# Kernel tuning notes

Hardware: AMD Instinct MI355X
Metric: run time of the kernel (lower is better)

## Reference

```python
import jax, jax.numpy as jnp
import numpy as np

B = 2048      # number of binary mixtures
NPM = 30      # atoms per molecule
N = B * NPM   # total nodes per side
EPM = 120     # directed edges per molecule
IN_DIM = 74
H = 128
NC = 2


def setup_inputs() -> dict:
    key = jax.random.key(0)
    ks = jax.random.split(key, 24)
    rng = np.random.default_rng(0)
    off = np.repeat(np.arange(B, dtype=np.int64) * NPM, EPM)
    mk_idx = lambda: jnp.asarray((rng.integers(0, NPM, B * EPM) + off).astype(np.int32))

    def lin(k, fi, fo):
        return (jax.random.normal(k, (fi, fo), jnp.float32) / np.sqrt(fi)).astype(jnp.float32)

    inp = {
        'h1': jax.random.normal(ks[0], (N, IN_DIM), jnp.float32),
        'h2': jax.random.normal(ks[1], (N, IN_DIM), jnp.float32),
        'solv1_x': jax.random.uniform(ks[2], (B,), jnp.float32),
        'inter_hb': jax.random.uniform(ks[3], (B,), jnp.float32),
        'intra_hb1': jax.random.uniform(ks[4], (B,), jnp.float32),
        'intra_hb2': jax.random.uniform(ks[5], (B,), jnp.float32),
        'Wg1': lin(ks[6], IN_DIM, H), 'bg1': jnp.zeros((H,), jnp.float32),
        'Wg2': lin(ks[7], H, H), 'bg2': jnp.zeros((H,), jnp.float32),
        'Wp': lin(ks[8], H, H), 'bp': jnp.zeros((H,), jnp.float32),
        'We1': lin(ks[9], 1, 32), 'be1': jnp.zeros((32,), jnp.float32),
        'We2': lin(ks[10], 32, H * H), 'be2': jnp.zeros((H * H,), jnp.float32),
        'bnn': jnp.zeros((H,), jnp.float32),
        'Wih': lin(ks[11], H, 3 * H), 'bih': jnp.zeros((3 * H,), jnp.float32),
        'Whh': lin(ks[12], H, 3 * H), 'bhh': jnp.zeros((3 * H,), jnp.float32),
        'Wcl1': lin(ks[13], 2 * H, H), 'bcl1': jnp.zeros((H,), jnp.float32),
        'Wcl2': lin(ks[14], H, H), 'bcl2': jnp.zeros((H,), jnp.float32),
        'Wcl3': lin(ks[15], H, NC), 'bcl3': jnp.zeros((NC,), jnp.float32),
        'src1': mk_idx(), 'dst1': mk_idx(), 'src2': mk_idx(), 'dst2': mk_idx(),
    }
    return inp


def _graphconv(x, src, dst, W, b, n):
    # DGL GraphConv, norm='both': D_in^{-1/2} A D_out^{-1/2} X W + b
    ones = jnp.ones(src.shape[0], x.dtype)
    d_out = jnp.maximum(jax.ops.segment_sum(ones, src, num_segments=n), 1.0)
    d_in = jnp.maximum(jax.ops.segment_sum(ones, dst, num_segments=n), 1.0)
    m = (x * jax.lax.rsqrt(d_out)[:, None])[src]
    agg = jax.ops.segment_sum(m, dst, num_segments=n)
    return (agg * jax.lax.rsqrt(d_in)[:, None]) @ W + b


def _gru_step(x, h, Wih, bih, Whh, bhh):
    gi = x @ Wih + bih
    gh = h @ Whh + bhh
    ir, iz, ih = jnp.split(gi, 3, axis=-1)
    hr, hz, hn = jnp.split(gh, 3, axis=-1)
    r = jax.nn.sigmoid(ir + hr)
    z = jax.nn.sigmoid(iz + hz)
    n = jnp.tanh(ih + r * hn)
    return (1.0 - z) * n + z * h


def _forward(h1, h2, solv1_x, inter_hb, intra_hb1, intra_hb2,
             Wg1, bg1, Wg2, bg2, Wp, bp, We1, be1, We2, be2, bnn,
             Wih, bih, Whh, bhh, Wcl1, bcl1, Wcl2, bcl2, Wcl3, bcl3,
             src1, dst1, src2, dst2):
    # shared GraphConv layers on both molecule graphs
    t1 = jax.nn.relu(_graphconv(h1, src1, dst1, Wg1, bg1, N))
    t1 = jax.nn.relu(_graphconv(t1, src1, dst1, Wg2, bg2, N))
    t2 = jax.nn.relu(_graphconv(h2, src2, dst2, Wg1, bg1, N))
    t2 = jax.nn.relu(_graphconv(t2, src2, dst2, Wg2, bg2, N))
    # dgl.mean_nodes: per-molecule mean (uniform NPM nodes per molecule)
    hg1 = t1.reshape(B, NPM, H).mean(axis=1) * solv1_x[:, None]
    hg2 = t2.reshape(B, NPM, H).mean(axis=1) * (1.0 - solv1_x)[:, None]
    x = jnp.concatenate([hg1, hg2], axis=0)  # (2B, H)

    # empty_solvsys: inter edges i<->i+B (both dirs) then self-loops
    ar = jnp.arange(B, dtype=jnp.int32)
    ss = jnp.concatenate([ar, ar + B, ar, ar + B])
    sd = jnp.concatenate([ar + B, ar, ar, ar + B])
    ef = jnp.concatenate([inter_hb, inter_hb, intra_hb1, intra_hb2])[:, None]  # (4B,1)

    # MPNNconv: project, NNConv(sum) + GRU, 1 message-passing step
    x = jax.nn.relu(x @ Wp + bp)
    hstate = x
    for _ in range(1):
        w = (jax.nn.relu(ef @ We1 + be1) @ We2 + be2).reshape(-1, H, H)  # (4B,H,H)
        msg = jnp.einsum('ed,edf->ef', x[ss], w)
        agg = jax.ops.segment_sum(msg, sd, num_segments=2 * B) + bnn
        x = _gru_step(jax.nn.relu(agg), hstate, Wih, bih, Whh, bhh)
        hstate = x

    hg = jnp.concatenate([x[:B], x[B:]], axis=1)  # (B, 2H)
    o = jax.nn.relu(hg @ Wcl1 + bcl1)
    o = jax.nn.relu(o @ Wcl2 + bcl2)
    return o @ Wcl3 + bcl3


def reference(h1, h2, solv1_x, inter_hb, intra_hb1, intra_hb2,
              Wg1, bg1, Wg2, bg2, Wp, bp, We1, be1, We2, be2, bnn,
              Wih, bih, Whh, bhh, Wcl1, bcl1, Wcl2, bcl2, Wcl3, bcl3,
              src1, dst1, src2, dst2):
    return _forward(h1, h2, solv1_x, inter_hb, intra_hb1, intra_hb2,
                    Wg1, bg1, Wg2, bg2, Wp, bp, We1, be1, We2, be2, bnn,
                    Wih, bih, Whh, bhh, Wcl1, bcl1, Wcl2, bcl2, Wcl3, bcl3,
                    src1, dst1, src2, dst2)
```

## Files before the change

kernel.cpp:

```cpp
#include <hip/hip_runtime.h>
#include <hip/hip_bf16.h>
#include <math.h>

#define B2    2048
#define NPM   30
#define EPM   120

typedef __attribute__((ext_vector_type(8))) short short8;
typedef __attribute__((ext_vector_type(4))) float f32x4;

__device__ __forceinline__ ushort f2bf(float x) {
  unsigned u = __float_as_uint(x);
  return (ushort)((u + 0x7FFFu + ((u >> 16) & 1u)) >> 16);
}
__device__ __forceinline__ float bf2f(ushort h) {
  return __uint_as_float(((unsigned)h) << 16);
}

__device__ __forceinline__ int swz128(int r, int kb) { return r * 128 + (kb ^ ((r & 7) << 4)); }
__device__ __forceinline__ int swz256(int r, int kb) { return r * 256 + (kb ^ ((r & 15) << 4)); }

struct PrepDescs {
  const float* W[8];
  ushort* hi[8];
  ushort* lo[8];
  int Kreal[8], Kpad[8], N[8];
  int blk0[9];
};

__global__ __launch_bounds__(256) void prep_all_kernel(PrepDescs d)
{
  int b = blockIdx.x;
  int di = 0;
  #pragma unroll
  for (int j = 1; j < 8; ++j) if (b >= d.blk0[j]) di = j;
  int idx = (b - d.blk0[di]) * 256 + threadIdx.x;
  int Kp8 = d.Kpad[di] >> 3;
  int tot = d.N[di] * Kp8;
  if (idx >= tot) return;
  int n = idx / Kp8;
  int k8 = (idx - n * Kp8) << 3;
  const float* W = d.W[di];
  ushort* hi = d.hi[di];
  ushort* lo = d.lo[di];
  int Kreal = d.Kreal[di], Kpad = d.Kpad[di], N = d.N[di];
  #pragma unroll
  for (int j = 0; j < 8; ++j) {
    int k = k8 + j;
    float x = (k < Kreal) ? W[(long)k * N + n] : 0.f;
    ushort h = f2bf(x);
    hi[(long)n * Kpad + k] = h;
    lo[(long)n * Kpad + k] = f2bf(x - bf2f(h));
  }
}

__global__ __launch_bounds__(256) void prep_we2_kernel(
    const float* __restrict__ We2, ushort* __restrict__ hi, ushort* __restrict__ lo)
{
  int idx = blockIdx.x * 256 + threadIdx.x;
  int k = idx >> 11;
  int rem = idx & 2047;
  int n = rem >> 4;
  int d8 = (rem & 15) << 3;
  #pragma unroll
  for (int j = 0; j < 8; ++j) {
    int d = d8 + j;
    float x = We2[k * 16384 + d * 128 + n];
    ushort h = f2bf(x);
    hi[k * 16384 + n * 128 + d] = h;
    lo[k * 16384 + n * 128 + d] = f2bf(x - bf2f(h));
  }
}

__global__ __launch_bounds__(256, 4) void grufuse_kernel(
    const float* __restrict__ aggA, const float* __restrict__ aggB,
    const float* __restrict__ zb, const float* __restrict__ bnn,
    const float* __restrict__ xp,
    const ushort* __restrict__ Wihh, const ushort* __restrict__ Wihl,
    const float* __restrict__ bih,
    const ushort* __restrict__ Whhh, const ushort* __restrict__ Whhl,
    const float* __restrict__ bhh,
    float* __restrict__ xnew)
{
  __shared__ __align__(16) char A1h[8192], A1l[8192];
  __shared__ __align__(16) char A2h[8192], A2l[8192];
  __shared__ __align__(16) char Bh[4096], Bl[4096];
  const int tid = threadIdx.x;
  const int w = tid >> 6, l = tid & 63;
  const int rt = blockIdx.x >> 2;
  const int qt = blockIdx.x & 3;
  const long rowBase = (long)rt * 32;
  const int rw = w & 1;
  const int cs = w >> 1;
  const int ar = rw * 16 + (l & 15);
  const int crow = rw * 16 + ((l >> 4) << 2);

  #pragma unroll
  for (int q = 0; q < 4; ++q) {
    int t = tid + 256 * q;
    int r = t >> 5, k4 = (t & 31) << 2;
    long gr = rowBase + r;
    long i = (gr < B2) ? gr : (gr - B2);
    float4 za = *(const float4*)&zb[i * 128 + k4];
    float4 zc = *(const float4*)&zb[(i + B2) * 128 + k4];
    float4 bn = *(const float4*)&bnn[k4];
    const float* ap = (gr < B2) ? &aggA[i * 128 + k4] : &aggB[i * 128 + k4];
    float4 ag = *(const float4*)ap;
    float4 xv;
    xv.x = fmaxf(ag.x + za.x + zc.x + bn.x, 0.f);
    xv.y = fmaxf(ag.y + za.y + zc.y + bn.y, 0.f);
    xv.z = fmaxf(ag.z + za.z + zc.z + bn.z, 0.f);
    xv.w = fmaxf(ag.w + za.w + zc.w + bn.w, 0.f);
    ushort4 h4, l4;
    h4.x = f2bf(xv.x); l4.x = f2bf(xv.x - bf2f(h4.x));
    h4.y = f2bf(xv.y); l4.y = f2bf(xv.y - bf2f(h4.y));
    h4.z = f2bf(xv.z); l4.z = f2bf(xv.z - bf2f(h4.z));
    h4.w = f2bf(xv.w); l4.w = f2bf(xv.w - bf2f(h4.w));
    *(ushort4*)(A1h + swz256(r, k4 * 2)) = h4;
    *(ushort4*)(A1l + swz256(r, k4 * 2)) = l4;
    float4 pv = *(const float4*)&xp[gr * 128 + k4];
    h4.x = f2bf(pv.x); l4.x = f2bf(pv.x - bf2f(h4.x));
    h4.y = f2bf(pv.y); l4.y = f2bf(pv.y - bf2f(h4.y));
    h4.z = f2bf(pv.z); l4.z = f2bf(pv.z - bf2f(h4.z));
    h4.w = f2bf(pv.w); l4.w = f2bf(pv.w - bf2f(h4.w));
    *(ushort4*)(A2h + swz256(r, k4 * 2)) = h4;
    *(ushort4*)(A2l + swz256(r, k4 * 2)) = l4;
  }
  __syncthreads();

  f32x4 rg = (f32x4){0,0,0,0}, zg = (f32x4){0,0,0,0};

  for (int gate = 0; gate < 3; ++gate) {
    f32x4 gi = (f32x4){0,0,0,0}, gh = (f32x4){0,0,0,0};
    for (int src = 0; src < 2; ++src) {
      const ushort* Wh = src ? Whhh : Wihh;
      const ushort* Wl = src ? Whhl : Wihl;
      const char* Ah = src ? A2h : A1h;
      const char* Al = src ? A2l : A1l;
      for (int k0 = 0; k0 < 128; k0 += 64) {
        __syncthreads();
        {
          int n = tid >> 3, k8 = (tid & 7) << 3;
          long wrow = (long)(gate * 128 + qt * 32 + n);
          *(uint4*)(Bh + swz128(n, k8 * 2)) = *(const uint4*)&Wh[wrow * 128 + k0 + k8];
          *(uint4*)(Bl + swz128(n, k8 * 2)) = *(const uint4*)&Wl[wrow * 128 + k0 + k8];
        }
        __syncthreads();
        f32x4 a = (src == 0) ? gi : gh;
        #pragma unroll
        for (int ks = 0; ks < 2; ++ks) {
          const int ko = ks * 32 + (l >> 4) * 8;
          short8 ah  = *(const short8*)(Ah + swz256(ar, (k0 + ko) * 2));
          short8 al8 = *(const short8*)(Al + swz256(ar, (k0 + ko) * 2));
          const int c = cs * 16 + (l & 15);
          short8 bh  = *(const short8*)(Bh + swz128(c, ko * 2));
          short8 bl8 = *(const short8*)(Bl + swz128(c, ko * 2));
          a = __builtin_amdgcn_mfma_f32_16x16x32_bf16(al8, bh, a, 0, 0, 0);
          a = __builtin_amdgcn_mfma_f32_16x16x32_bf16(ah, bl8, a, 0, 0, 0);
          a = __builtin_amdgcn_mfma_f32_16x16x32_bf16(ah, bh, a, 0, 0, 0);
        }
        if (src == 0) gi = a; else gh = a;
      }
    }
    int cg = qt * 32 + cs * 16 + (l & 15);
    float bi = bih[gate * 128 + cg], bh2 = bhh[gate * 128 + cg];
    #pragma unroll
    for (int i = 0; i < 4; ++i) {
      float a = gi[i] + bi;
      float b = gh[i] + bh2;
      if (gate == 0) {
        rg[i] = 1.f / (1.f + expf(-(a + b)));
      } else if (gate == 1) {
        zg[i] = 1.f / (1.f + expf(-(a + b)));
      } else {
        float ng = tanhf(a + rg[i] * b);
        long row = rowBase + crow + i;
        float h = xp[row * 128 + cg];
        xnew[row * 128 + cg] = (1.f - zg[i]) * ng + zg[i] * h;
      }
    }
  }
}

__global__ __launch_bounds__(256) void xpzb_kernel(
    const float* __restrict__ xcat,
    const ushort* __restrict__ Wph, const ushort* __restrict__ Wpl,
    const float* __restrict__ bp,
    const ushort* __restrict__ be2h, const ushort* __restrict__ be2l,
    float* __restrict__ xp, float* __restrict__ zb)
{
  __shared__ __align__(16) char AhB[16384], AlB[16384];
  __shared__ __align__(16) char BhB[16384], BlB[16384];
  const int tid = threadIdx.x;
  const int w = tid >> 6, l = tid & 63;
  const long rowBase = (long)blockIdx.x * 64;
  const int ar = w * 16 + (l & 15);
  const int crow = w * 16 + ((l >> 4) << 2);

  #pragma unroll
  for (int q = 0; q < 8; ++q) {
    int t = tid + 256 * q;
    int r = t >> 5, k4 = (t & 31) << 2;
    float4 v = *(const float4*)&xcat[(rowBase + r) * 128 + k4];
    ushort4 h4, l4;
    h4.x = f2bf(v.x); l4.x = f2bf(v.x - bf2f(h4.x));
    h4.y = f2bf(v.y); l4.y = f2bf(v.y - bf2f(h4.y));
    h4.z = f2bf(v.z); l4.z = f2bf(v.z - bf2f(h4.z));
    h4.w = f2bf(v.w); l4.w = f2bf(v.w - bf2f(h4.w));
    *(ushort4*)(AhB + swz256(r, k4 * 2)) = h4;
    *(ushort4*)(AlB + swz256(r, k4 * 2)) = l4;
  }
  __syncthreads();

  f32x4 acc[8];
  #pragma unroll
  for (int fc = 0; fc < 8; ++fc) acc[fc] = (f32x4){0.f, 0.f, 0.f, 0.f};
  for (int k0 = 0; k0 < 128; k0 += 64) {
    #pragma unroll
    for (int q = 0; q < 4; ++q) {
      int lin = tid + 256 * q;
      int n = lin >> 3, k8 = (lin & 7) << 3;
      *(uint4*)(BhB + swz128(n, k8 * 2)) = *(const uint4*)&Wph[n * 128 + k0 + k8];
      *(uint4*)(BlB + swz128(n, k8 * 2)) = *(const uint4*)&Wpl[n * 128 + k0 + k8];
    }
    __syncthreads();
    #pragma unroll
    for (int ks = 0; ks < 2; ++ks) {
      const int ko = ks * 32 + (l >> 4) * 8;
      short8 ah  = *(const short8*)(AhB + swz256(ar, (k0 + ko) * 2));
      short8 al8 = *(const short8*)(AlB + swz256(ar, (k0 + ko) * 2));
      #pragma unroll
      for (int fc = 0; fc < 8; ++fc) {
        const int c = fc * 16 + (l & 15);
        short8 bh  = *(const short8*)(BhB + swz128(c, ko * 2));
        short8 bl8 = *(const short8*)(BlB + swz128(c, ko * 2));
        acc[fc] = __builtin_amdgcn_mfma_f32_16x16x32_bf16(al8, bh, acc[fc], 0, 0, 0);
        acc[fc] = __builtin_amdgcn_mfma_f32_16x16x32_bf16(ah, bl8, acc[fc], 0, 0, 0);
        acc[fc] = __builtin_amdgcn_mfma_f32_16x16x32_bf16(ah, bh, acc[fc], 0, 0, 0);
      }
    }
    __syncthreads();
  }

  #pragma unroll
  for (int fc = 0; fc < 8; ++fc) {
    int col = fc * 16 + (l & 15);
    float bv = bp[col];
    #pragma unroll
    for (int i = 0; i < 4; ++i) {
      int lr = crow + i;
      float v = fmaxf(acc[fc][i] + bv, 0.f);
      xp[(rowBase + lr) * 128 + col] = v;
      ushort h = f2bf(v);
      *(ushort*)(AhB + swz256(lr, col * 2)) = h;
      *(ushort*)(AlB + swz256(lr, col * 2)) = f2bf(v - bf2f(h));
    }
  }

  #pragma unroll
  for (int fc = 0; fc < 8; ++fc) acc[fc] = (f32x4){0.f, 0.f, 0.f, 0.f};
  for (int k0 = 0; k0 < 128; k0 += 64) {
    __syncthreads();
    #pragma unroll
    for (int q = 0; q < 4; ++q) {
      int lin = tid + 256 * q;
      int n = lin >> 3, k8 = (lin & 7) << 3;
      *(uint4*)(BhB + swz128(n, k8 * 2)) = *(const uint4*)&be2h[n * 128 + k0 + k8];
      *(uint4*)(BlB + swz128(n, k8 * 2)) = *(const uint4*)&be2l[n * 128 + k0 + k8];
    }
    __syncthreads();
    #pragma unroll
    for (int ks = 0; ks < 2; ++ks) {
      const int ko = ks * 32 + (l >> 4) * 8;
      short8 ah  = *(const short8*)(AhB + swz256(ar, (k0 + ko) * 2));
      short8 al8 = *(const short8*)(AlB + swz256(ar, (k0 + ko) * 2));
      #pragma unroll
      for (int fc = 0; fc < 8; ++fc) {
        const int c = fc * 16 + (l & 15);
        short8 bh  = *(const short8*)(BhB + swz128(c, ko * 2));
        short8 bl8 = *(const short8*)(BlB + swz128(c, ko * 2));
        acc[fc] = __builtin_amdgcn_mfma_f32_16x16x32_bf16(al8, bh, acc[fc], 0, 0, 0);
        acc[fc] = __builtin_amdgcn_mfma_f32_16x16x32_bf16(ah, bl8, acc[fc], 0, 0, 0);
        acc[fc] = __builtin_amdgcn_mfma_f32_16x16x32_bf16(ah, bh, acc[fc], 0, 0, 0);
      }
    }
  }
  #pragma unroll
  for (int fc = 0; fc < 8; ++fc) {
    int col = fc * 16 + (l & 15);
    #pragma unroll
    for (int i = 0; i < 4; ++i) {
      int lr = crow + i;
      zb[(rowBase + lr) * 128 + col] = acc[fc][i];
    }
  }
}

__global__ __launch_bounds__(256) void cls_kernel(
    const float* __restrict__ xnew,
    const ushort* __restrict__ W1h, const ushort* __restrict__ W1l,
    const float* __restrict__ b1,
    const ushort* __restrict__ W2h, const ushort* __restrict__ W2l,
    const float* __restrict__ b2,
    const float* __restrict__ Wcl3, const float* __restrict__ bcl3,
    float* __restrict__ out)
{
  __shared__ __align__(16) char O1h[16384], O1l[16384];
  __shared__ __align__(16) char AhB[8192], AlB[8192];
  __shared__ __align__(16) char BhB[16384], BlB[16384];
  const int tid = threadIdx.x;
  const int w = tid >> 6, l = tid & 63;
  const long rowBase = (long)blockIdx.x * 64;
  const int ar = w * 16 + (l & 15);
  const int crow = w * 16 + ((l >> 4) << 2);

  f32x4 acc[8];
  #pragma unroll
  for (int fc = 0; fc < 8; ++fc) acc[fc] = (f32x4){0.f, 0.f, 0.f, 0.f};
  for (int k0 = 0; k0 < 256; k0 += 64) {
    const float* Ab = (k0 < 128) ? xnew : (xnew + (long)B2 * 128);
    const int kc = k0 & 127;
    #pragma unroll
    for (int q = 0; q < 4; ++q) {
      int lin = tid + 256 * q;
      int r = lin >> 4, k4 = (lin & 15) << 2;
      float4 v = *(const float4*)&Ab[(rowBase + r) * 128 + kc + k4];
      ushort4 h4, l4;
      h4.x = f2bf(v.x); l4.x = f2bf(v.x - bf2f(h4.x));
      h4.y = f2bf(v.y); l4.y = f2bf(v.y - bf2f(h4.y));
      h4.z = f2bf(v.z); l4.z = f2bf(v.z - bf2f(h4.z));
      h4.w = f2bf(v.w); l4.w = f2bf(v.w - bf2f(h4.w));
      *(ushort4*)(AhB + swz128(r, k4 * 2)) = h4;
      *(ushort4*)(AlB + swz128(r, k4 * 2)) = l4;
    }
    #pragma unroll
    for (int q = 0; q < 4; ++q) {
      int lin = tid + 256 * q;
      int n = lin >> 3, k8 = (lin & 7) << 3;
      *(uint4*)(BhB + swz128(n, k8 * 2)) = *(const uint4*)&W1h[(long)n * 256 + k0 + k8];
      *(uint4*)(BlB + swz128(n, k8 * 2)) = *(const uint4*)&W1l[(long)n * 256 + k0 + k8];
    }
    __syncthreads();
    #pragma unroll
    for (int ks = 0; ks < 2; ++ks) {
      const int ko = ks * 32 + (l >> 4) * 8;
      short8 ah  = *(const short8*)(AhB + swz128(ar, ko * 2));
      short8 al8 = *(const short8*)(AlB + swz128(ar, ko * 2));
      #pragma unroll
      for (int fc = 0; fc < 8; ++fc) {
        const int c = fc * 16 + (l & 15);
        short8 bh  = *(const short8*)(BhB + swz128(c, ko * 2));
        short8 bl8 = *(const short8*)(BlB + swz128(c, ko * 2));
        acc[fc] = __builtin_amdgcn_mfma_f32_16x16x32_bf16(al8, bh, acc[fc], 0, 0, 0);
        acc[fc] = __builtin_amdgcn_mfma_f32_16x16x32_bf16(ah, bl8, acc[fc], 0, 0, 0);
        acc[fc] = __builtin_amdgcn_mfma_f32_16x16x32_bf16(ah, bh, acc[fc], 0, 0, 0);
      }
    }
    __syncthreads();
  }
  #pragma unroll
  for (int fc = 0; fc < 8; ++fc) {
    int col = fc * 16 + (l & 15);
    float bv = b1[col];
    #pragma unroll
    for (int i = 0; i < 4; ++i) {
      int lr = crow + i;
      float v = fmaxf(acc[fc][i] + bv, 0.f);
      ushort h = f2bf(v);
      *(ushort*)(O1h + swz256(lr, col * 2)) = h;
      *(ushort*)(O1l + swz256(lr, col * 2)) = f2bf(v - bf2f(h));
    }
  }

  #pragma unroll
  for (int fc = 0; fc < 8; ++fc) acc[fc] = (f32x4){0.f, 0.f, 0.f, 0.f};
  for (int k0 = 0; k0 < 128; k0 += 64) {
    __syncthreads();
    #pragma unroll
    for (int q = 0; q < 4; ++q) {
      int lin = tid + 256 * q;
      int n = lin >> 3, k8 = (lin & 7) << 3;
      *(uint4*)(BhB + swz128(n, k8 * 2)) = *(const uint4*)&W2h[n * 128 + k0 + k8];
      *(uint4*)(BlB + swz128(n, k8 * 2)) = *(const uint4*)&W2l[n * 128 + k0 + k8];
    }
    __syncthreads();
    #pragma unroll
    for (int ks = 0; ks < 2; ++ks) {
      const int ko = ks * 32 + (l >> 4) * 8;
      short8 ah  = *(const short8*)(O1h + swz256(ar, (k0 + ko) * 2));
      short8 al8 = *(const short8*)(O1l + swz256(ar, (k0 + ko) * 2));
      #pragma unroll
      for (int fc = 0; fc < 8; ++fc) {
        const int c = fc * 16 + (l & 15);
        short8 bh  = *(const short8*)(BhB + swz128(c, ko * 2));
        short8 bl8 = *(const short8*)(BlB + swz128(c, ko * 2));
        acc[fc] = __builtin_amdgcn_mfma_f32_16x16x32_bf16(al8, bh, acc[fc], 0, 0, 0);
        acc[fc] = __builtin_amdgcn_mfma_f32_16x16x32_bf16(ah, bl8, acc[fc], 0, 0, 0);
        acc[fc] = __builtin_amdgcn_mfma_f32_16x16x32_bf16(ah, bh, acc[fc], 0, 0, 0);
      }
    }
  }

  float p0[4] = {0.f, 0.f, 0.f, 0.f}, p1[4] = {0.f, 0.f, 0.f, 0.f};
  #pragma unroll
  for (int fc = 0; fc < 8; ++fc) {
    int col = fc * 16 + (l & 15);
    float bv = b2[col];
    float w0 = Wcl3[col * 2], w1 = Wcl3[col * 2 + 1];
    #pragma unroll
    for (int i = 0; i < 4; ++i) {
      float v = fmaxf(acc[fc][i] + bv, 0.f);
      p0[i] = fmaf(v, w0, p0[i]);
      p1[i] = fmaf(v, w1, p1[i]);
    }
  }
  #pragma unroll
  for (int i = 0; i < 4; ++i) {
    #pragma unroll
    for (int m = 1; m < 16; m <<= 1) {
      p0[i] += __shfl_xor(p0[i], m);
      p1[i] += __shfl_xor(p1[i], m);
    }
    if ((l & 15) == 0) {
      long row = rowBase + crow + i;
      out[row * 2 + 0] = p0[i] + bcl3[0];
      out[row * 2 + 1] = p1[i] + bcl3[1];
    }
  }
}

__global__ __launch_bounds__(256, 1) void zfold_mfma_kernel(
    const float* __restrict__ xp,
    const ushort* __restrict__ We2h, const ushort* __restrict__ We2l,
    const float* __restrict__ interhb, const float* __restrict__ ia1,
    const float* __restrict__ ia2, const float* __restrict__ We1,
    const float* __restrict__ be1,
    float* __restrict__ aggA, float* __restrict__ aggB)
{
  __shared__ __align__(16) ushort Ah[2][64 * 72], Al[2][64 * 72];
  __shared__ __align__(16) ushort Bh[128 * 72], Bl[128 * 72];
  __shared__ float accAs[32 * 128], accBs[32 * 128];
  __shared__ float ehs[3][32][8];
  const int tid = threadIdx.x;
  const int w = tid >> 6, l = tid & 63;
  const int rg = blockIdx.x >> 2, kq = blockIdx.x & 3;
  const int i0 = rg * 32;

  for (int t = tid; t < 2048; t += 256) {
    int r = t >> 5, k4 = (t & 31) << 2;
    int gr = (r < 32) ? (i0 + r) : (B2 + i0 + r - 32);
    float4 v = *(const float4*)&xp[(long)gr * 128 + k4];
    int ch = k4 >> 6, ko = k4 & 63;
    ushort4 h4, l4;
    h4.x = f2bf(v.x); l4.x = f2bf(v.x - bf2f(h4.x));
    h4.y = f2bf(v.y); l4.y = f2bf(v.y - bf2f(h4.y));
    h4.z = f2bf(v.z); l4.z = f2bf(v.z - bf2f(h4.z));
    h4.w = f2bf(v.w); l4.w = f2bf(v.w - bf2f(h4.w));
    *(ushort4*)&Ah[ch][r * 72 + ko] = h4;
    *(ushort4*)&Al[ch][r * 72 + ko] = l4;
  }
  for (int t = tid; t < 768; t += 256) {
    int grp = t >> 8, rem = t & 255;
    int mm = rem >> 3, kk = rem & 7;
    int k = kq * 8 + kk;
    float u = (grp == 0) ? interhb[i0 + mm] : (grp == 1) ? ia1[i0 + mm] : ia2[i0 + mm];
    ehs[grp][mm][kk] = fmaxf(fmaf(u, We1[k], be1[k]), 0.f);
  }
  for (int t = tid; t < 4096; t += 256) { accAs[t] = 0.f; accBs[t] = 0.f; }

  float foldA[8][4] = {{0.f}}, foldB[8][4] = {{0.f}};
  const int ar = w * 16 + (l & 15);

  for (int kk = 0; kk < 8; ++kk) {
    const int k = kq * 8 + kk;
    f32x4 acc[8];
    #pragma unroll
    for (int fc = 0; fc < 8; ++fc) acc[fc] = (f32x4){0.f, 0.f, 0.f, 0.f};
    for (int ch = 0; ch < 2; ++ch) {
      __syncthreads();
      #pragma unroll
      for (int q = 0; q < 4; ++q) {
        int lin = tid + 256 * q;
        int n = lin >> 3, k8 = (lin & 7) << 3;
        *(uint4*)&Bh[n * 72 + k8] = *(const uint4*)&We2h[k * 16384 + n * 128 + ch * 64 + k8];
        *(uint4*)&Bl[n * 72 + k8] = *(const uint4*)&We2l[k * 16384 + n * 128 + ch * 64 + k8];
      }
      __syncthreads();
      #pragma unroll
      for (int ks = 0; ks < 2; ++ks) {
        const int ko = ks * 32 + (l >> 4) * 8;
        short8 ah  = *(const short8*)&Ah[ch][ar * 72 + ko];
        short8 al8 = *(const short8*)&Al[ch][ar * 72 + ko];
        #pragma unroll
        for (int fc = 0; fc < 8; ++fc) {
          const int c = fc * 16 + (l & 15);
          short8 bh  = *(const short8*)&Bh[c * 72 + ko];
          short8 bl8 = *(const short8*)&Bl[c * 72 + ko];
          acc[fc] = __builtin_amdgcn_mfma_f32_16x16x32_bf16(al8, bh, acc[fc], 0, 0, 0);
          acc[fc] = __builtin_amdgcn_mfma_f32_16x16x32_bf16(ah, bl8, acc[fc], 0, 0, 0);
          acc[fc] = __builtin_amdgcn_mfma_f32_16x16x32_bf16(ah, bh, acc[fc], 0, 0, 0);
        }
      }
    }
    #pragma unroll
    for (int i = 0; i < 4; ++i) {
      int lr = w * 16 + ((l >> 4) << 2) + i;
      int m = lr & 31, up = lr >> 5;
      float eA = up ? ehs[0][m][kk] : ehs[1][m][kk];
      float eB = up ? ehs[2][m][kk] : ehs[0][m][kk];
      #pragma unroll
      for (int fc = 0; fc < 8; ++fc) {
        foldA[fc][i] = fmaf(eA, acc[fc][i], foldA[fc][i]);
        foldB[fc][i] = fmaf(eB, acc[fc][i], foldB[fc][i]);
      }
    }
  }
  #pragma unroll
  for (int i = 0; i < 4; ++i) {
    int lr = w * 16 + ((l >> 4) << 2) + i;
    int m = lr & 31;
    #pragma unroll
    for (int fc = 0; fc < 8; ++fc) {
      int c = fc * 16 + (l & 15);
      atomicAdd(&accAs[m * 128 + c], foldA[fc][i]);
      atomicAdd(&accBs[m * 128 + c], foldB[fc][i]);
    }
  }
  __syncthreads();
  for (int t = tid; t < 4096; t += 256) {
    int mm = t >> 7, c = t & 127;
    atomicAdd(&aggA[(long)(i0 + mm) * 128 + c], accAs[t]);
    atomicAdd(&aggB[(long)(i0 + mm) * 128 + c], accBs[t]);
  }
}

__global__ __launch_bounds__(256) void adj_kernel(
    const int* __restrict__ src1, const int* __restrict__ dst1,
    const int* __restrict__ src2, const int* __restrict__ dst2,
    float* __restrict__ Abuf)
{
  __shared__ float cnt[4][30 * 33];
  __shared__ float rsOa[4][32], rsIa[4][32];
  const int tid = threadIdx.x, wid = tid >> 6, lane = tid & 63;
  const int gm = blockIdx.x * 4 + wid;
  const int g = gm >> 11, m = gm & 2047;
  const int* src = g ? src2 : src1;
  const int* dst = g ? dst2 : dst1;

  for (int i = lane; i < 30 * 33; i += 64) cnt[wid][i] = 0.f;
  __syncthreads();
  for (int e = lane; e < EPM; e += 64) {
    int s = src[m * EPM + e] - m * NPM;
    int d = dst[m * EPM + e] - m * NPM;
    atomicAdd(&cnt[wid][d * 33 + s], 1.0f);
  }
  __syncthreads();
  if (lane < NPM) {
    float sum = 0.f;
    for (int s = 0; s < NPM; ++s) sum += cnt[wid][lane * 33 + s];
    rsIa[wid][lane] = rsqrtf(fmaxf(sum, 1.f));
  } else if (lane >= 32 && lane < 32 + NPM) {
    int s = lane - 32; float sum = 0.f;
    for (int d = 0; d < NPM; ++d) sum += cnt[wid][d * 33 + s];
    rsOa[wid][s] = rsqrtf(fmaxf(sum, 1.f));
  }
  __syncthreads();
  const long base = (long)gm * 960;
  for (int i = lane; i < 960; i += 64) {
    int d = i >> 5, s = i & 31;
    float v = (d < NPM && s < NPM)
            ? cnt[wid][d * 33 + s] * rsIa[wid][d] * rsOa[wid][s] : 0.f;
    Abuf[base + i] = v;
  }
}

__global__ __launch_bounds__(512, 4) void gconv_kernel(
    const float* __restrict__ h1, const float* __restrict__ h2,
    const float* __restrict__ Abuf, const float* __restrict__ bg1,
    const ushort* __restrict__ W1h, const ushort* __restrict__ W1l,
    const ushort* __restrict__ W2h, const ushort* __restrict__ W2l,
    const float* __restrict__ bias2, const float* __restrict__ s1x,
    float* __restrict__ xcat)
{
  __shared__ __align__(16) char pool[66560];
  char* AhB = pool;
  char* AlB = pool + 16384;
  char* BhB = pool + 32768;
  char* BlB = pool + 49152;
  char* A2h = pool;
  char* A2l = pool + 8192;
  char* Byh = pool + 32768;
  char* Byl = pool + 49152;
  float* cs = (float*)(pool + 65536);

  const int tid = threadIdx.x;
  const int p = blockIdx.x;
  const int g = p >> 10;
  const int mloc = (p & 1023) * 2;
  const float* hsrc = g ? h2 : h1;
  if (tid < 256) cs[tid] = 0.f;

  const int w8 = tid >> 6, l = tid & 63;
  const int rw = w8 & 3;
  const int ch2 = w8 >> 2;
  const int ar = rw * 16 + (l & 15);
  const int crow = rw * 16 + ((l >> 4) << 2);

  #pragma unroll
  for (int q = 0; q < 4; ++q) {
    int lin = tid + 512 * q;
    int r = lin >> 5, k4 = (lin & 31) << 2;
    float4 v = make_float4(0.f, 0.f, 0.f, 0.f);
    if (r < 60) {
      const float* Ar = &hsrc[(long)(mloc * 30 + r) * 74];
      if (k4 + 4 <= 74) {
        float2 a = *(const float2*)&Ar[k4];
        float2 b = *(const float2*)&Ar[k4 + 2];
        v = make_float4(a.x, a.y, b.x, b.y);
      } else if (k4 + 2 <= 74) {
        float2 a = *(const float2*)&Ar[k4];
        v.x = a.x; v.y = a.y;
      }
    }
    ushort4 h4, l4;
    h4.x = f2bf(v.x); l4.x = f2bf(v.x - bf2f(h4.x));
    h4.y = f2bf(v.y); l4.y = f2bf(v.y - bf2f(h4.y));
    h4.z = f2bf(v.z); l4.z = f2bf(v.z - bf2f(h4.z));
    h4.w = f2bf(v.w); l4.w = f2bf(v.w - bf2f(h4.w));
    *(ushort4*)(AhB + swz256(r, k4 * 2)) = h4;
    *(ushort4*)(AlB + swz256(r, k4 * 2)) = l4;
  }
  __syncthreads();

  f32x4 acc[4];
  #pragma unroll
  for (int fc = 0; fc < 4; ++fc) acc[fc] = (f32x4){0.f, 0.f, 0.f, 0.f};
  for (int k0 = 0; k0 < 128; k0 += 64) {
    #pragma unroll
    for (int q = 0; q < 2; ++q) {
      int lin = tid + 512 * q;
      int n = lin >> 3, k8 = (lin & 7) << 3;
      *(uint4*)(BhB + swz128(n, k8 * 2)) = *(const uint4*)&W1h[n * 128 + k0 + k8];
      *(uint4*)(BlB + swz128(n, k8 * 2)) = *(const uint4*)&W1l[n * 128 + k0 + k8];
    }
    __syncthreads();
    #pragma unroll
    for (int ks = 0; ks < 2; ++ks) {
      const int ko = ks * 32 + (l >> 4) * 8;
      short8 ah  = *(const short8*)(AhB + swz256(ar, (k0 + ko) * 2));
      short8 al8 = *(const short8*)(AlB + swz256(ar, (k0 + ko) * 2));
      #pragma unroll
      for (int fc = 0; fc < 4; ++fc) {
        const int c = ch2 * 64 + fc * 16 + (l & 15);
        short8 bh  = *(const short8*)(BhB + swz128(c, ko * 2));
        short8 bl8 = *(const short8*)(BlB + swz128(c, ko * 2));
        acc[fc] = __builtin_amdgcn_mfma_f32_16x16x32_bf16(al8, bh, acc[fc], 0, 0, 0);
        acc[fc] = __builtin_amdgcn_mfma_f32_16x16x32_bf16(ah, bl8, acc[fc], 0, 0, 0);
        acc[fc] = __builtin_amdgcn_mfma_f32_16x16x32_bf16(ah, bh, acc[fc], 0, 0, 0);
      }
    }
    __syncthreads();
  }

  {
    const long ab0 = (long)(g * 2048 + mloc) * 960;
    for (int t = tid; t < 4096; t += 512) {
      int row = t >> 6, k = t & 63;
      float v = 0.f;
      if (row < 30) { if (k < 30) v = Abuf[ab0 + row * 32 + k]; }
      else if (row < 60) { if (k >= 30 && k < 60) v = Abuf[ab0 + 960 + (row - 30) * 32 + (k - 30)]; }
      ushort h = f2bf(v);
      *(ushort*)(A2h + swz128(row, k * 2)) = h;
      *(ushort*)(A2l + swz128(row, k * 2)) = f2bf(v - bf2f(h));
    }
  }
  #pragma unroll
  for (int fc = 0; fc < 4; ++fc) {
    int n = ch2 * 64 + fc * 16 + (l & 15);
    ushort4 h4, l4;
    h4.x = f2bf(acc[fc][0]); l4.x = f2bf(acc[fc][0] - bf2f(h4.x));
    h4.y = f2bf(acc[fc][1]); l4.y = f2bf(acc[fc][1] - bf2f(h4.y));
    h4.z = f2bf(acc[fc][2]); l4.z = f2bf(acc[fc][2] - bf2f(h4.z));
    h4.w = f2bf(acc[fc][3]); l4.w = f2bf(acc[fc][3] - bf2f(h4.w));
    *(ushort4*)(Byh + swz128(n, crow * 2)) = h4;
    *(ushort4*)(Byl + swz128(n, crow * 2)) = l4;
  }
  __syncthreads();

  f32x4 acc2[4];
  #pragma unroll
  for (int fc = 0; fc < 4; ++fc) acc2[fc] = (f32x4){0.f, 0.f, 0.f, 0.f};
  #pragma unroll
  for (int ks = 0; ks < 2; ++ks) {
    const int ko = ks * 32 + (l >> 4) * 8;
    short8 ah  = *(const short8*)(A2h + swz128(ar, ko * 2));
    short8 al8 = *(const short8*)(A2l + swz128(ar, ko * 2));
    #pragma unroll
    for (int fc = 0; fc < 4; ++fc) {
      const int c = ch2 * 64 + fc * 16 + (l & 15);
      short8 bh  = *(const short8*)(Byh + swz128(c, ko * 2));
      short8 bl8 = *(const short8*)(Byl + swz128(c, ko * 2));
      acc2[fc] = __builtin_amdgcn_mfma_f32_16x16x32_bf16(al8, bh, acc2[fc], 0, 0, 0);
      acc2[fc] = __builtin_amdgcn_mfma_f32_16x16x32_bf16(ah, bl8, acc2[fc], 0, 0, 0);
      acc2[fc] = __builtin_amdgcn_mfma_f32_16x16x32_bf16(ah, bh, acc2[fc], 0, 0, 0);
    }
  }
  __syncthreads();

  #pragma unroll
  for (int fc = 0; fc < 4; ++fc) {
    int n = ch2 * 64 + fc * 16 + (l & 15);
    float bv = bg1[n];
    float t0 = fmaxf(acc2[fc][0] + bv, 0.f);
    float t1v = fmaxf(acc2[fc][1] + bv, 0.f);
    float t2v = fmaxf(acc2[fc][2] + bv, 0.f);
    float t3 = fmaxf(acc2[fc][3] + bv, 0.f);
    ushort4 h4, l4;
    h4.x = f2bf(t0); l4.x = f2bf(t0 - bf2f(h4.x));
    h4.y = f2bf(t1v); l4.y = f2bf(t1v - bf2f(h4.y));
    h4.z = f2bf(t2v); l4.z = f2bf(t2v - bf2f(h4.z));
    h4.w = f2bf(t3); l4.w = f2bf(t3 - bf2f(h4.w));
    *(ushort4*)(Byh + swz128(n, crow * 2)) = h4;
    *(ushort4*)(Byl + swz128(n, crow * 2)) = l4;
  }
  __syncthreads();

  #pragma unroll
  for (int fc = 0; fc < 4; ++fc) acc2[fc] = (f32x4){0.f, 0.f, 0.f, 0.f};
  #pragma unroll
  for (int ks = 0; ks < 2; ++ks) {
    const int ko = ks * 32 + (l >> 4) * 8;
    short8 ah  = *(const short8*)(A2h + swz128(ar, ko * 2));
    short8 al8 = *(const short8*)(A2l + swz128(ar, ko * 2));
    #pragma unroll
    for (int fc = 0; fc < 4; ++fc) {
      const int c = ch2 * 64 + fc * 16 + (l & 15);
      short8 bh  = *(const short8*)(Byh + swz128(c, ko * 2));
      short8 bl8 = *(const short8*)(Byl + swz128(c, ko * 2));
      acc2[fc] = __builtin_amdgcn_mfma_f32_16x16x32_bf16(al8, bh, acc2[fc], 0, 0, 0);
      acc2[fc] = __builtin_amdgcn_mfma_f32_16x16x32_bf16(ah, bl8, acc2[fc], 0, 0, 0);
      acc2[fc] = __builtin_amdgcn_mfma_f32_16x16x32_bf16(ah, bh, acc2[fc], 0, 0, 0);
    }
  }
  __syncthreads();

  #pragma unroll
  for (int fc = 0; fc < 4; ++fc) {
    int n = ch2 * 64 + fc * 16 + (l & 15);
    #pragma unroll
    for (int i = 0; i < 4; ++i) {
      int r = crow + i;
      ushort h = f2bf(acc2[fc][i]);
      *(ushort*)(AhB + swz256(r, n * 2)) = h;
      *(ushort*)(AlB + swz256(r, n * 2)) = f2bf(acc2[fc][i] - bf2f(h));
    }
  }

  #pragma unroll
  for (int fc = 0; fc < 4; ++fc) acc[fc] = (f32x4){0.f, 0.f, 0.f, 0.f};
  for (int k0 = 0; k0 < 128; k0 += 64) {
    __syncthreads();
    #pragma unroll
    for (int q = 0; q < 2; ++q) {
      int lin = tid + 512 * q;
      int n = lin >> 3, k8 = (lin & 7) << 3;
      *(uint4*)(BhB + swz128(n, k8 * 2)) = *(const uint4*)&W2h[n * 128 + k0 + k8];
      *(uint4*)(BlB + swz128(n, k8 * 2)) = *(const uint4*)&W2l[n * 128 + k0 + k8];
    }
    __syncthreads();
    #pragma unroll
    for (int ks = 0; ks < 2; ++ks) {
      const int ko = ks * 32 + (l >> 4) * 8;
      short8 ah  = *(const short8*)(AhB + swz256(ar, (k0 + ko) * 2));
      short8 al8 = *(const short8*)(AlB + swz256(ar, (k0 + ko) * 2));
      #pragma unroll
      for (int fc = 0; fc < 4; ++fc) {
        const int c = ch2 * 64 + fc * 16 + (l & 15);
        short8 bh  = *(const short8*)(BhB + swz128(c, ko * 2));
        short8 bl8 = *(const short8*)(BlB + swz128(c, ko * 2));
        acc[fc] = __builtin_amdgcn_mfma_f32_16x16x32_bf16(al8, bh, acc[fc], 0, 0, 0);
        acc[fc] = __builtin_amdgcn_mfma_f32_16x16x32_bf16(ah, bl8, acc[fc], 0, 0, 0);
        acc[fc] = __builtin_amdgcn_mfma_f32_16x16x32_bf16(ah, bh, acc[fc], 0, 0, 0);
      }
    }
  }
  __syncthreads();

  #pragma unroll
  for (int fc = 0; fc < 4; ++fc) {
    int col = ch2 * 64 + fc * 16 + (l & 15);
    float bv = bias2[col];
    float s0 = 0.f, s1 = 0.f;
    #pragma unroll
    for (int i = 0; i < 4; ++i) {
      int lr = crow + i;
      if (lr < 60) {
        float v = fmaxf(acc[fc][i] + bv, 0.f);
        if (lr < NPM) s0 += v; else s1 += v;
      }
    }
    s0 += __shfl_down(s0, 32); s0 += __shfl_down(s0, 16);
    s1 += __shfl_down(s1, 32); s1 += __shfl_down(s1, 16);
    if ((l >> 4) == 0) {
      atomicAdd(&cs[col], s0);
      atomicAdd(&cs[128 + col], s1);
    }
  }
  __syncthreads();
  if (tid < 256) {
    int moll = tid >> 7, c = tid & 127;
    int gm = p * 2 + moll;
    int gg = gm >> 11, mm = gm & 2047;
    float sf = gg ? (1.f - s1x[mm]) : s1x[mm];
    xcat[(long)gm * 128 + c] = cs[moll * 128 + c] * (1.f / 30.f) * sf;
  }
}

extern "C" void kernel_launch(void* const* d_in, const int* in_sizes, int n_in,
                              void* d_out, int out_size, void* d_ws, size_t ws_size,
                              hipStream_t stream)
{
  const float* h1   = (const float*)d_in[0];
  const float* h2   = (const float*)d_in[1];
  const float* s1x  = (const float*)d_in[2];
  const float* ihb  = (const float*)d_in[3];
  const float* ia1  = (const float*)d_in[4];
  const float* ia2  = (const float*)d_in[5];
  const float* Wg1  = (const float*)d_in[6];
  const float* bg1  = (const float*)d_in[7];
  const float* Wg2  = (const float*)d_in[8];
  const float* bg2  = (const float*)d_in[9];
  const float* Wp   = (const float*)d_in[10];
  const float* bp   = (const float*)d_in[11];
  const float* We1  = (const float*)d_in[12];
  const float* be1  = (const float*)d_in[13];
  const float* We2  = (const float*)d_in[14];
  const float* be2  = (const float*)d_in[15];
  const float* bnn  = (const float*)d_in[16];
  const float* Wih  = (const float*)d_in[17];
  const float* bih  = (const float*)d_in[18];
  const float* Whh  = (const float*)d_in[19];
  const float* bhh  = (const float*)d_in[20];
  const float* Wcl1 = (const float*)d_in[21];
  const float* bcl1 = (const float*)d_in[22];
  const float* Wcl2 = (const float*)d_in[23];
  const float* bcl2 = (const float*)d_in[24];
  const float* Wcl3 = (const float*)d_in[25];
  const float* bcl3 = (const float*)d_in[26];
  const int*   src1 = (const int*)d_in[27];
  const int*   dst1 = (const int*)d_in[28];
  const int*   src2 = (const int*)d_in[29];
  const int*   dst2 = (const int*)d_in[30];
  float* out = (float*)d_out;
  float* ws  = (float*)d_ws;

  float* Abuf = ws;
  float* dwn  = ws + 35389440;

  float* xcat = dwn;
  float* xp   = dwn + 524288;
  float* zb   = dwn + 1048576;
  float* aggA = dwn + 1572864;
  float* aggB = dwn + 1835008;
  float* xnew = dwn + 2097152;

  ushort* wt     = (ushort*)(dwn + 6815744);
  ushort* WpTh   = wt;               ushort* WpTl   = wt + 16384;
  ushort* be2Th  = wt + 32768;       ushort* be2Tl  = wt + 49152;
  ushort* WihTh  = wt + 65536;       ushort* WihTl  = wt + 114688;
  ushort* WhhTh  = wt + 163840;      ushort* WhhTl  = wt + 212992;
  ushort* Wcl1Th = wt + 262144;      ushort* Wcl1Tl = wt + 294912;
  ushort* Wcl2Th = wt + 327680;      ushort* Wcl2Tl = wt + 344064;
  ushort* Wg1Th  = wt + 360448;      ushort* Wg1Tl  = wt + 376832;
  ushort* Wg2Th  = wt + 393216;      ushort* Wg2Tl  = wt + 409600;
  ushort* We2h   = wt + 425984;      ushort* We2l   = wt + 950272;

  PrepDescs pd;
  const float* Ws_[8]  = {Wp, be2, Wih, Whh, Wcl1, Wcl2, Wg1, Wg2};
  ushort* his[8]       = {WpTh, be2Th, WihTh, WhhTh, Wcl1Th, Wcl2Th, Wg1Th, Wg2Th};
  ushort* los[8]       = {WpTl, be2Tl, WihTl, WhhTl, Wcl1Tl, Wcl2Tl, Wg1Tl, Wg2Tl};
  int kr[8]   = {128, 128, 128, 128, 256, 128, 74, 128};
  int kp[8]   = {128, 128, 128, 128, 256, 128, 128, 128};
  int nn[8]   = {128, 128, 384, 384, 128, 128, 128, 128};
  int acc_blk = 0;
  for (int i = 0; i < 8; ++i) {
    pd.W[i] = Ws_[i]; pd.hi[i] = his[i]; pd.lo[i] = los[i];
    pd.Kreal[i] = kr[i]; pd.Kpad[i] = kp[i]; pd.N[i] = nn[i];
    pd.blk0[i] = acc_blk;
    acc_blk += (nn[i] * (kp[i] >> 3) + 255) / 256;
  }
  pd.blk0[8] = acc_blk;
  prep_all_kernel<<<acc_blk, 256, 0, stream>>>(pd);
  prep_we2_kernel<<<256, 256, 0, stream>>>(We2, We2h, We2l);

  adj_kernel<<<1024, 256, 0, stream>>>(src1, dst1, src2, dst2, Abuf);
  gconv_kernel<<<2048, 512, 0, stream>>>(h1, h2, Abuf, bg1, Wg1Th, Wg1Tl,
                                         Wg2Th, Wg2Tl, bg2, s1x, xcat);

  xpzb_kernel<<<64, 256, 0, stream>>>(xcat, WpTh, WpTl, bp, be2Th, be2Tl, xp, zb);
  hipMemsetAsync(aggA, 0, 2 * 262144 * sizeof(float), stream);
  zfold_mfma_kernel<<<256, 256, 0, stream>>>(xp, We2h, We2l, ihb, ia1, ia2,
                                             We1, be1, aggA, aggB);
  grufuse_kernel<<<512, 256, 0, stream>>>(aggA, aggB, zb, bnn, xp,
                                          WihTh, WihTl, bih, WhhTh, WhhTl, bhh,
                                          xnew);
  cls_kernel<<<32, 256, 0, stream>>>(xnew, Wcl1Th, Wcl1Tl, bcl1,
                                     Wcl2Th, Wcl2Tl, bcl2, Wcl3, bcl3, out);
}
```

Baseline: 181.6 us.

## Split zfold K range across more blocks, alias LDS, hoist A fragments to registers

```diff
diff --git a/kernel.cpp b/kernel.cpp
--- a/kernel.cpp
+++ b/kernel.cpp
@@ -429,7 +429,7 @@
   }
 }
 
-__global__ __launch_bounds__(256, 1) void zfold_mfma_kernel(
+__global__ __launch_bounds__(256, 2) void zfold_mfma_kernel(
     const float* __restrict__ xp,
     const ushort* __restrict__ We2h, const ushort* __restrict__ We2l,
     const float* __restrict__ interhb, const float* __restrict__ ia1,
@@ -437,14 +437,20 @@
     const float* __restrict__ be1,
     float* __restrict__ aggA, float* __restrict__ aggB)
 {
-  __shared__ __align__(16) ushort Ah[2][64 * 72], Al[2][64 * 72];
-  __shared__ __align__(16) ushort Bh[128 * 72], Bl[128 * 72];
-  __shared__ float accAs[32 * 128], accBs[32 * 128];
-  __shared__ float ehs[3][32][8];
+  __shared__ __align__(16) char poolz[76800];
+  ushort* AhP = (ushort*)poolz;
+  ushort* AlP = (ushort*)(poolz + 18432);
+  float* accAs = (float*)poolz;
+  float* accBs = (float*)(poolz + 16384);
+  ushort* Bh = (ushort*)(poolz + 36864);
+  ushort* Bl = (ushort*)(poolz + 55296);
+  float (*ehs)[32][4] = (float(*)[32][4])(poolz + 73728);
+
   const int tid = threadIdx.x;
   const int w = tid >> 6, l = tid & 63;
-  const int rg = blockIdx.x >> 2, kq = blockIdx.x & 3;
+  const int rg = blockIdx.x >> 3, kq = blockIdx.x & 7;
   const int i0 = rg * 32;
+  const int ar = w * 16 + (l & 15);
 
   for (int t = tid; t < 2048; t += 256) {
     int r = t >> 5, k4 = (t & 31) << 2;
@@ -456,23 +462,34 @@
     h4.y = f2bf(v.y); l4.y = f2bf(v.y - bf2f(h4.y));
     h4.z = f2bf(v.z); l4.z = f2bf(v.z - bf2f(h4.z));
     h4.w = f2bf(v.w); l4.w = f2bf(v.w - bf2f(h4.w));
-    *(ushort4*)&Ah[ch][r * 72 + ko] = h4;
-    *(ushort4*)&Al[ch][r * 72 + ko] = l4;
-  }
-  for (int t = tid; t < 768; t += 256) {
-    int grp = t >> 8, rem = t & 255;
-    int mm = rem >> 3, kk = rem & 7;
-    int k = kq * 8 + kk;
+    *(ushort4*)&AhP[ch * 4608 + r * 72 + ko] = h4;
+    *(ushort4*)&AlP[ch * 4608 + r * 72 + ko] = l4;
+  }
+  for (int t = tid; t < 384; t += 256) {
+    int grp = t >> 7, rem = t & 127;
+    int mm = rem >> 2, kk = rem & 3;
+    int k = kq * 4 + kk;
     float u = (grp == 0) ? interhb[i0 + mm] : (grp == 1) ? ia1[i0 + mm] : ia2[i0 + mm];
     ehs[grp][mm][kk] = fmaxf(fmaf(u, We1[k], be1[k]), 0.f);
   }
-  for (int t = tid; t < 4096; t += 256) { accAs[t] = 0.f; accBs[t] = 0.f; }
+  __syncthreads();
+
+  short8 ahr[2][2], alr[2][2];
+  #pragma unroll
+  for (int ch = 0; ch < 2; ++ch)
+    #pragma unroll
+    for (int ks = 0; ks < 2; ++ks) {
+      int ko = ks * 32 + (l >> 4) * 8;
+      ahr[ch][ks] = *(const short8*)&AhP[ch * 4608 + ar * 72 + ko];
+      alr[ch][ks] = *(const short8*)&AlP[ch * 4608 + ar * 72 + ko];
+    }
+  __syncthreads();
+  for (int t = tid; t < 8192; t += 256) ((float*)poolz)[t] = 0.f;
 
   float foldA[8][4] = {{0.f}}, foldB[8][4] = {{0.f}};
-  const int ar = w * 16 + (l & 15);
-
-  for (int kk = 0; kk < 8; ++kk) {
-    const int k = kq * 8 + kk;
+
+  for (int kk = 0; kk < 4; ++kk) {
+    const int k = kq * 4 + kk;
     f32x4 acc[8];
     #pragma unroll
     for (int fc = 0; fc < 8; ++fc) acc[fc] = (f32x4){0.f, 0.f, 0.f, 0.f};
@@ -489,8 +506,8 @@
       #pragma unroll
       for (int ks = 0; ks < 2; ++ks) {
         const int ko = ks * 32 + (l >> 4) * 8;
-        short8 ah  = *(const short8*)&Ah[ch][ar * 72 + ko];
-        short8 al8 = *(const short8*)&Al[ch][ar * 72 + ko];
+        short8 ah  = ahr[ch][ks];
+        short8 al8 = alr[ch][ks];
         #pragma unroll
         for (int fc = 0; fc < 8; ++fc) {
           const int c = fc * 16 + (l & 15);
@@ -515,6 +532,7 @@
       }
     }
   }
+  __syncthreads();
   #pragma unroll
   for (int i = 0; i < 4; ++i) {
     int lr = w * 16 + ((l >> 4) << 2) + i;
@@ -899,7 +917,7 @@
 
   xpzb_kernel<<<64, 256, 0, stream>>>(xcat, WpTh, WpTl, bp, be2Th, be2Tl, xp, zb);
   hipMemsetAsync(aggA, 0, 2 * 262144 * sizeof(float), stream);
-  zfold_mfma_kernel<<<256, 256, 0, stream>>>(xp, We2h, We2l, ihb, ia1, ia2,
+  zfold_mfma_kernel<<<512, 256, 0, stream>>>(xp, We2h, We2l, ihb, ia1, ia2,
                                              We1, be1, aggA, aggB);
   grufuse_kernel<<<512, 256, 0, stream>>>(aggA, aggB, zb, bnn, xp,
                                           WihTh, WihTl, bih, WhhTh, WhhTl, bhh,
```

Result: slower. 197.9 us (+9.0%).

## Fuse normalized adjacency construction into graph-conv kernel, dropping global Abuf

Applied to the files above, without the earlier changes.

```diff
diff --git a/kernel.cpp b/kernel.cpp
--- a/kernel.cpp
+++ b/kernel.cpp
@@ -534,49 +534,11 @@
   }
 }
 
-__global__ __launch_bounds__(256) void adj_kernel(
+__global__ __launch_bounds__(512, 4) void gconv_kernel(
+    const float* __restrict__ h1, const float* __restrict__ h2,
     const int* __restrict__ src1, const int* __restrict__ dst1,
     const int* __restrict__ src2, const int* __restrict__ dst2,
-    float* __restrict__ Abuf)
-{
-  __shared__ float cnt[4][30 * 33];
-  __shared__ float rsOa[4][32], rsIa[4][32];
-  const int tid = threadIdx.x, wid = tid >> 6, lane = tid & 63;
-  const int gm = blockIdx.x * 4 + wid;
-  const int g = gm >> 11, m = gm & 2047;
-  const int* src = g ? src2 : src1;
-  const int* dst = g ? dst2 : dst1;
-
-  for (int i = lane; i < 30 * 33; i += 64) cnt[wid][i] = 0.f;
-  __syncthreads();
-  for (int e = lane; e < EPM; e += 64) {
-    int s = src[m * EPM + e] - m * NPM;
-    int d = dst[m * EPM + e] - m * NPM;
-    atomicAdd(&cnt[wid][d * 33 + s], 1.0f);
-  }
-  __syncthreads();
-  if (lane < NPM) {
-    float sum = 0.f;
-    for (int s = 0; s < NPM; ++s) sum += cnt[wid][lane * 33 + s];
-    rsIa[wid][lane] = rsqrtf(fmaxf(sum, 1.f));
-  } else if (lane >= 32 && lane < 32 + NPM) {
-    int s = lane - 32; float sum = 0.f;
-    for (int d = 0; d < NPM; ++d) sum += cnt[wid][d * 33 + s];
-    rsOa[wid][s] = rsqrtf(fmaxf(sum, 1.f));
-  }
-  __syncthreads();
-  const long base = (long)gm * 960;
-  for (int i = lane; i < 960; i += 64) {
-    int d = i >> 5, s = i & 31;
-    float v = (d < NPM && s < NPM)
-            ? cnt[wid][d * 33 + s] * rsIa[wid][d] * rsOa[wid][s] : 0.f;
-    Abuf[base + i] = v;
-  }
-}
-
-__global__ __launch_bounds__(512, 4) void gconv_kernel(
-    const float* __restrict__ h1, const float* __restrict__ h2,
-    const float* __restrict__ Abuf, const float* __restrict__ bg1,
+    const float* __restrict__ bg1,
     const ushort* __restrict__ W1h, const ushort* __restrict__ W1l,
     const ushort* __restrict__ W2h, const ushort* __restrict__ W2l,
     const float* __restrict__ bias2, const float* __restrict__ s1x,
@@ -592,6 +554,9 @@
   char* Byh = pool + 32768;
   char* Byl = pool + 49152;
   float* cs = (float*)(pool + 65536);
+  float* cntS = (float*)(pool + 16384);
+  float* rsIS = (float*)(pool + 24576);
+  float* rsOS = (float*)(pool + 24832);
 
   const int tid = threadIdx.x;
   const int p = blockIdx.x;
@@ -662,18 +627,6 @@
     __syncthreads();
   }
 
-  {
-    const long ab0 = (long)(g * 2048 + mloc) * 960;
-    for (int t = tid; t < 4096; t += 512) {
-      int row = t >> 6, k = t & 63;
-      float v = 0.f;
-      if (row < 30) { if (k < 30) v = Abuf[ab0 + row * 32 + k]; }
-      else if (row < 60) { if (k >= 30 && k < 60) v = Abuf[ab0 + 960 + (row - 30) * 32 + (k - 30)]; }
-      ushort h = f2bf(v);
-      *(ushort*)(A2h + swz128(row, k * 2)) = h;
-      *(ushort*)(A2l + swz128(row, k * 2)) = f2bf(v - bf2f(h));
-    }
-  }
   #pragma unroll
   for (int fc = 0; fc < 4; ++fc) {
     int n = ch2 * 64 + fc * 16 + (l & 15);
@@ -684,6 +637,47 @@
     h4.w = f2bf(acc[fc][3]); l4.w = f2bf(acc[fc][3] - bf2f(h4.w));
     *(ushort4*)(Byh + swz128(n, crow * 2)) = h4;
     *(ushort4*)(Byl + swz128(n, crow * 2)) = l4;
+  }
+  for (int t = tid; t < 2176; t += 512) ((float*)(pool + 16384))[t] = 0.f;
+  __syncthreads();
+
+  if (tid < 2 * EPM) {
+    int mol = tid / EPM, e = tid - mol * EPM;
+    const int* srcp = g ? src2 : src1;
+    const int* dstp = g ? dst2 : dst1;
+    int m = mloc + mol;
+    int s = srcp[m * EPM + e] - m * NPM;
+    int d = dstp[m * EPM + e] - m * NPM;
+    atomicAdd(&cntS[mol * 990 + d * 33 + s], 1.0f);
+  }
+  __syncthreads();
+
+  if (tid < 60) {
+    int mol = tid / 30, r = tid - mol * 30;
+    float s = 0.f;
+    for (int k = 0; k < 30; ++k) s += cntS[mol * 990 + r * 33 + k];
+    rsIS[mol * 32 + r] = rsqrtf(fmaxf(s, 1.f));
+  } else if (tid >= 64 && tid < 124) {
+    int t2 = tid - 64;
+    int mol = t2 / 30, sc = t2 - mol * 30;
+    float s = 0.f;
+    for (int d = 0; d < 30; ++d) s += cntS[mol * 990 + d * 33 + sc];
+    rsOS[mol * 32 + sc] = rsqrtf(fmaxf(s, 1.f));
+  }
+  __syncthreads();
+
+  for (int t = tid; t < 4096; t += 512) {
+    int row = t >> 6, k = t & 63;
+    float v = 0.f;
+    if (row < 30) {
+      if (k < 30) v = cntS[row * 33 + k] * rsIS[row] * rsOS[k];
+    } else if (row < 60) {
+      if (k >= 30 && k < 60)
+        v = cntS[990 + (row - 30) * 33 + (k - 30)] * rsIS[32 + row - 30] * rsOS[32 + k - 30];
+    }
+    ushort h = f2bf(v);
+    *(ushort*)(A2h + swz128(row, k * 2)) = h;
+    *(ushort*)(A2l + swz128(row, k * 2)) = f2bf(v - bf2f(h));
   }
   __syncthreads();
 
@@ -854,7 +848,6 @@
   float* out = (float*)d_out;
   float* ws  = (float*)d_ws;
 
-  float* Abuf = ws;
   float* dwn  = ws + 35389440;
 
   float* xcat = dwn;
@@ -893,9 +886,9 @@
   prep_all_kernel<<<acc_blk, 256, 0, stream>>>(pd);
   prep_we2_kernel<<<256, 256, 0, stream>>>(We2, We2h, We2l);
 
-  adj_kernel<<<1024, 256, 0, stream>>>(src1, dst1, src2, dst2, Abuf);
-  gconv_kernel<<<2048, 512, 0, stream>>>(h1, h2, Abuf, bg1, Wg1Th, Wg1Tl,
-                                         Wg2Th, Wg2Tl, bg2, s1x, xcat);
+  gconv_kernel<<<2048, 512, 0, stream>>>(h1, h2, src1, dst1, src2, dst2,
+                                         bg1, Wg1Th, Wg1Tl, Wg2Th, Wg2Tl,
+                                         bg2, s1x, xcat);
 
   xpzb_kernel<<<64, 256, 0, stream>>>(xcat, WpTh, WpTl, bp, be2Th, be2Tl, xp, zb);
   hipMemsetAsync(aggA, 0, 2 * 262144 * sizeof(float), stream);
```

New measurement: 174.3 us. -4.0%, faster.
